# Performance work log

Hardware: AMD Instinct MI355X
Metric: run time of the kernel (lower is better)

Reference implementation:

```python
import jax, jax.numpy as jnp
import numpy as np
import math

N_HEADS = 8

def setup_inputs() -> dict:
    key = jax.random.key(0)
    qkv = jax.random.normal(key, (4, 1536, 2048), dtype=jnp.float32)
    return {"qkv": qkv}

def reference(qkv):
    bs, width, length = qkv.shape
    ch = width // (3 * N_HEADS)
    # reshape to [bs*n_heads, 3*ch, length] then split into q, k, v
    qkv_h = qkv.reshape(bs * N_HEADS, 3 * ch, length)
    q = qkv_h[:, :ch]
    k = qkv_h[:, ch:2 * ch]
    v = qkv_h[:, 2 * ch:]
    scale = 1.0 / math.sqrt(math.sqrt(ch))
    # scores: [B*H, T, S]
    weight = jnp.einsum('bct,bcs->bts', q * scale, k * scale)
    weight = jax.nn.softmax(weight.astype(jnp.float32), axis=-1).astype(weight.dtype)
    a = jnp.einsum('bts,bcs->bct', weight, v)  # [B*H, ch, T]
    return a.reshape(bs, N_HEADS * ch, length)
```

## Files before the change

### kernel.cpp

```cpp
#include <hip/hip_runtime.h>
#include <hip/hip_bf16.h>

typedef __attribute__((ext_vector_type(8))) short bf16x8;
typedef __attribute__((ext_vector_type(8))) unsigned short u16x8;
typedef __attribute__((ext_vector_type(4))) float f32x4;
typedef __attribute__((ext_vector_type(16))) float f32x16;

#define SEQ 2048
#define NBH 32
#define QSCALE 0.1803368801111204f

#if __has_builtin(__builtin_amdgcn_exp2f)
#define EXP2(x) __builtin_amdgcn_exp2f(x)
#else
#define EXP2(x) exp2f(x)
#endif

__device__ __forceinline__ unsigned short bfc(float f) {
  union { __hip_bfloat16 h; unsigned short u; } v;
  v.h = __float2bfloat16(f);
  return v.u;
}

__device__ __forceinline__ void gl_lds16(const void* g, void* l) {
  __builtin_amdgcn_global_load_lds((__attribute__((address_space(1))) void*)g,
                                   (__attribute__((address_space(3))) void*)l, 16, 0, 0);
}

__global__ __launch_bounds__(256)
void prep_kernel(const float* __restrict__ qkv, unsigned short* __restrict__ ws) {
  const int tid = threadIdx.x;
  const int b = blockIdx.x;
  if (b < 4096) {
    int gid = b * 256 + tid;
    int sec = gid >> 19;
    int r = gid & 524287;
    int bh = r >> 14;
    int rr = r & 16383;
    int cc = rr >> 11;
    int t = rr & 2047;
    const float* src = qkv + ((size_t)(bh >> 3) * 1536 + (bh & 7) * 192 + sec * 64 + cc * 8) * SEQ + t;
    const float scale = sec ? 1.0f : QSCALE;
    u16x8 o;
    #pragma unroll
    for (int e = 0; e < 8; ++e) o[e] = bfc(src[(size_t)e * SEQ] * scale);
    unsigned short* dst = ws + ((size_t)sec * NBH * SEQ + (size_t)bh * SEQ + t) * 64;
    *(u16x8*)(dst + ((cc ^ (t & 7)) * 8)) = o;
  } else {
    int cid = (b - 4096) * 256 + tid;
    int bh = cid >> 14;
    int rr = cid & 16383;
    int c = rr >> 8;
    int cc = rr & 255;
    int grp = cc >> 3, sub = cc & 7;
    const float* src = qkv + ((size_t)(bh >> 3) * 1536 + (bh & 7) * 192 + 128 + c) * SEQ + cc * 8;
    float4 a = *(const float4*)(src);
    float4 bv = *(const float4*)(src + 4);
    u16x8 o;
    o[0] = bfc(a.x); o[1] = bfc(a.y); o[2] = bfc(a.z); o[3] = bfc(a.w);
    o[4] = bfc(bv.x); o[5] = bfc(bv.y); o[6] = bfc(bv.z); o[7] = bfc(bv.w);
    unsigned short* dst = ws + (size_t)2 * NBH * SEQ * 64 +
                          ((size_t)bh * 64 + c) * SEQ + grp * 64 + ((sub ^ (c & 7)) * 8);
    *(u16x8*)dst = o;
  }
}

__global__ __launch_bounds__(256, 2)
void attn_main(const unsigned short* __restrict__ ws, float* __restrict__ out) {
  const int bid = blockIdx.x;
  const int bh = (bid & 7) + 8 * ((bid >> 3) >> 4);
  const int tile = (bid >> 3) & 15;
  const int t0 = tile * 128;

  const unsigned short* Qws = ws + ((size_t)bh * SEQ + t0) * 64;
  const unsigned short* Kws = ws + (size_t)NBH * SEQ * 64 + (size_t)bh * SEQ * 64;
  const unsigned short* Vws = ws + (size_t)2 * NBH * SEQ * 64 + (size_t)bh * 64 * SEQ;
  float* __restrict__ outb = out + (size_t)bh * 64 * SEQ;

  __shared__ __align__(16) char smem[32768];
  unsigned short* KtB = (unsigned short*)smem;
  unsigned short* VtB = (unsigned short*)(smem + 16384);

  const int tid = threadIdx.x;
  const int w = tid >> 6;
  const int ts = w & 1;
  const int sh = w >> 1;
  const int l = tid & 63;
  const int lw = l & 31;
  const int h = l >> 5;
  const int sw = lw & 7;

  bf16x8 qB[2][4];
  #pragma unroll
  for (int tsub = 0; tsub < 2; ++tsub) {
    const int rloc = ts * 64 + tsub * 32 + lw;
    #pragma unroll
    for (int kc = 0; kc < 4; ++kc)
      qB[tsub][kc] = *(const bf16x8*)&Qws[rloc * 64 + (((2 * kc + h) ^ sw) * 8)];
  }

  const int vc = tid >> 3, vj = tid & 7;
  const int vc2 = vc + 32;

  gl_lds16(Kws + (size_t)tid * 8, &KtB[tid * 8]);
  gl_lds16(Kws + (size_t)(tid + 256) * 8, &KtB[(tid + 256) * 8]);
  gl_lds16(Vws + (size_t)vc * SEQ + vj * 8, &VtB[tid * 8]);
  gl_lds16(Vws + (size_t)vc2 * SEQ + vj * 8, &VtB[(tid + 256) * 8]);
  __syncthreads();

  f32x16 zero16;
  #pragma unroll
  for (int i = 0; i < 16; ++i) zero16[i] = 0.f;
  bf16x8 onesB;
  #pragma unroll
  for (int i = 0; i < 8; ++i) onesB[i] = (short)0x3F80;

  f32x16 accO[2][2];
  f32x16 psum[2];
  accO[0][0] = zero16; accO[0][1] = zero16;
  accO[1][0] = zero16; accO[1][1] = zero16;
  psum[0] = zero16; psum[1] = zero16;

  int cur = 0;
  #pragma unroll 1
  for (int it = 0; it < SEQ / 64; ++it) {
    {
      const int s1 = (it + 1) & 31;
      const unsigned short* kn = Kws + (size_t)s1 * 4096;
      unsigned short* kd = KtB + (cur ^ 1) * 4096;
      gl_lds16(kn + (size_t)tid * 8, &kd[tid * 8]);
      gl_lds16(kn + (size_t)(tid + 256) * 8, &kd[(tid + 256) * 8]);
      unsigned short* vd = VtB + (cur ^ 1) * 4096;
      gl_lds16(Vws + (size_t)vc * SEQ + s1 * 64 + vj * 8, &vd[tid * 8]);
      gl_lds16(Vws + (size_t)vc2 * SEQ + s1 * 64 + vj * 8, &vd[(tid + 256) * 8]);
    }

    const unsigned short* kb = KtB + cur * 4096;
    const unsigned short* vb = VtB + cur * 4096;

    f32x16 accS[2];
    #pragma unroll
    for (int kc = 0; kc < 4; ++kc) {
      bf16x8 ka = *(const bf16x8*)&kb[(sh * 32 + lw) * 64 + (((2 * kc + h) ^ sw) * 8)];
      #pragma unroll
      for (int tsub = 0; tsub < 2; ++tsub)
        accS[tsub] = __builtin_amdgcn_mfma_f32_32x32x16_bf16(
            ka, qB[tsub][kc], kc ? accS[tsub] : zero16, 0, 0, 0);
    }

    #pragma unroll
    for (int tsub = 0; tsub < 2; ++tsub)
      #pragma unroll
      for (int r = 0; r < 16; ++r) accS[tsub][r] = EXP2(accS[tsub][r]);

    bf16x8 pA[2][2];
    #pragma unroll
    for (int tsub = 0; tsub < 2; ++tsub) {
      unsigned int pk[8];
      #pragma unroll
      for (int wd = 0; wd < 8; ++wd)
        asm("v_cvt_pk_bf16_f32 %0, %1, %2"
            : "=v"(pk[wd]) : "v"(accS[tsub][2 * wd]), "v"(accS[tsub][2 * wd + 1]));
      #pragma unroll
      for (int a = 0; a < 2; ++a) {
        unsigned int x0 = pk[4 * a + 0], y0 = pk[4 * a + 2];
        unsigned int x1 = pk[4 * a + 1], y1 = pk[4 * a + 3];
        asm("v_permlane32_swap_b32 %0, %1" : "+v"(x0), "+v"(y0));
        asm("v_permlane32_swap_b32 %0, %1" : "+v"(x1), "+v"(y1));
        union { unsigned int u[4]; bf16x8 v; } uu;
        uu.u[0] = x0; uu.u[1] = x1; uu.u[2] = y0; uu.u[3] = y1;
        pA[tsub][a] = uu.v;
      }
    }

    #pragma unroll
    for (int tsub = 0; tsub < 2; ++tsub)
      #pragma unroll
      for (int ks = 0; ks < 2; ++ks)
        psum[tsub] = __builtin_amdgcn_mfma_f32_32x32x16_bf16(pA[tsub][ks], onesB, psum[tsub], 0, 0, 0);

    #pragma unroll
    for (int ch = 0; ch < 2; ++ch) {
      #pragma unroll
      for (int ks = 0; ks < 2; ++ks) {
        bf16x8 vB = *(const bf16x8*)&vb[(32 * ch + lw) * 64 + (((sh * 4 + 2 * ks + h) ^ sw) * 8)];
        #pragma unroll
        for (int tsub = 0; tsub < 2; ++tsub)
          accO[tsub][ch] = __builtin_amdgcn_mfma_f32_32x32x16_bf16(pA[tsub][ks], vB, accO[tsub][ch], 0, 0, 0);
      }
    }

    __syncthreads();
    cur ^= 1;
  }

  float* red = (float*)smem;
  if (sh == 1) {
    #pragma unroll
    for (int tsub = 0; tsub < 2; ++tsub)
      #pragma unroll
      for (int ch = 0; ch < 2; ++ch)
        #pragma unroll
        for (int r = 0; r < 16; ++r)
          red[(((ts * 2 + tsub) * 2 + ch) * 16 + r) * 64 + l] = accO[tsub][ch][r];
  }
  __syncthreads();
  if (sh == 0) {
    #pragma unroll
    for (int tsub = 0; tsub < 2; ++tsub)
      #pragma unroll
      for (int ch = 0; ch < 2; ++ch)
        #pragma unroll
        for (int r = 0; r < 16; ++r)
          accO[tsub][ch][r] += red[(((ts * 2 + tsub) * 2 + ch) * 16 + r) * 64 + l];
  }
  __syncthreads();
  if (sh == 1) {
    #pragma unroll
    for (int tsub = 0; tsub < 2; ++tsub)
      #pragma unroll
      for (int r = 0; r < 16; ++r)
        red[((ts * 2 + tsub) * 16 + r) * 64 + l] = psum[tsub][r];
  }
  __syncthreads();
  if (sh == 0) {
    #pragma unroll
    for (int tsub = 0; tsub < 2; ++tsub) {
      float linv[16];
      #pragma unroll
      for (int r = 0; r < 16; ++r)
        linv[r] = 1.0f / (psum[tsub][r] + red[((ts * 2 + tsub) * 16 + r) * 64 + l]);
      #pragma unroll
      for (int ch = 0; ch < 2; ++ch) {
        #pragma unroll
        for (int r = 0; r < 16; ++r) {
          const int tg = t0 + ts * 64 + tsub * 32 + (r & 3) + 8 * (r >> 2) + 4 * h;
          outb[(size_t)(32 * ch + lw) * SEQ + tg] = accO[tsub][ch][r] * linv[r];
        }
      }
    }
  }
}

#define PAD 72
#define BTF 128
__device__ __forceinline__ unsigned short f2bf(float f) {
  union { float f; unsigned u; } v; v.f = f;
  return (unsigned short)((v.u + 0x7fffu + ((v.u >> 16) & 1u)) >> 16);
}

__global__ __launch_bounds__(512, 4)
void qkv_attn_fallback(const float* __restrict__ qkv, float* __restrict__ out) {
  const int bid = blockIdx.x;
  const int xcd = bid & 7;
  const int slot = bid >> 3;
  const int bh = xcd + 8 * (slot >> 4);
  const int tile = slot & 15;
  const int t0 = tile * BTF;

  const float* __restrict__ base = qkv + (size_t)((bh >> 3) * 1536 + (bh & 7) * 192) * SEQ;
  const float* __restrict__ qg = base;
  const float* __restrict__ kg = base + 64 * SEQ;
  const float* __restrict__ vg = base + 128 * SEQ;
  float* __restrict__ outb = out + (size_t)bh * 64 * SEQ;

  __shared__ __align__(16) unsigned short Qt[BTF * PAD];
  __shared__ __align__(16) unsigned short Kt[64 * PAD];
  __shared__ __align__(16) unsigned short Vt[64 * PAD];
  __shared__ __align__(16) unsigned short Pl[BTF * PAD];

  const int tid = threadIdx.x;
  const int w = tid >> 6;
  const int l = tid & 63;
  const int lr = l & 15;
  const int g = l >> 4;

  {
    const int cb = tid >> 5, tb = tid & 31;
    const int c0 = cb * 4, tt0 = tb * 4;
    const float* p = qg + c0 * SEQ + t0 + tt0;
    float4 r0 = *(const float4*)(p);
    float4 r1 = *(const float4*)(p + SEQ);
    float4 r2 = *(const float4*)(p + 2 * SEQ);
    float4 r3 = *(const float4*)(p + 3 * SEQ);
    const float s = 0.125f;
    ushort4 w0 = { f2bf(r0.x*s), f2bf(r1.x*s), f2bf(r2.x*s), f2bf(r3.x*s) };
    ushort4 w1 = { f2bf(r0.y*s), f2bf(r1.y*s), f2bf(r2.y*s), f2bf(r3.y*s) };
    ushort4 w2 = { f2bf(r0.z*s), f2bf(r1.z*s), f2bf(r2.z*s), f2bf(r3.z*s) };
    ushort4 w3 = { f2bf(r0.w*s), f2bf(r1.w*s), f2bf(r2.w*s), f2bf(r3.w*s) };
    *(ushort4*)&Qt[(tt0 + 0) * PAD + c0] = w0;
    *(ushort4*)&Qt[(tt0 + 1) * PAD + c0] = w1;
    *(ushort4*)&Qt[(tt0 + 2) * PAD + c0] = w2;
    *(ushort4*)&Qt[(tt0 + 3) * PAD + c0] = w3;
  }
  __syncthreads();

  bf16x8 qB0 = *(const bf16x8*)&Qt[(w * 16 + lr) * PAD + g * 8];
  bf16x8 qB1 = *(const bf16x8*)&Qt[(w * 16 + lr) * PAD + g * 8 + 32];

  f32x4 pv[4];
  #pragma unroll
  for (int i = 0; i < 4; ++i) pv[i] = (f32x4){0.f, 0.f, 0.f, 0.f};
  float mrun = -1e30f;
  float lsum = 0.f;

  for (int s0 = 0; s0 < SEQ; s0 += 64) {
    __syncthreads();
    {
      const int cb = tid >> 4, sb = tid & 15;
      const int c0 = cb * 2, sl = sb * 4;
      const float* p0 = kg + c0 * SEQ + s0 + sl;
      float4 a0 = *(const float4*)(p0);
      float4 a1 = *(const float4*)(p0 + SEQ);
      ushort2 y0 = { f2bf(a0.x), f2bf(a1.x) };
      ushort2 y1 = { f2bf(a0.y), f2bf(a1.y) };
      ushort2 y2 = { f2bf(a0.z), f2bf(a1.z) };
      ushort2 y3 = { f2bf(a0.w), f2bf(a1.w) };
      *(ushort2*)&Kt[(sl + 0) * PAD + c0] = y0;
      *(ushort2*)&Kt[(sl + 1) * PAD + c0] = y1;
      *(ushort2*)&Kt[(sl + 2) * PAD + c0] = y2;
      *(ushort2*)&Kt[(sl + 3) * PAD + c0] = y3;
    }
    {
      const int c = tid >> 3;
      const int sq = (tid & 7) * 8;
      const float* p0 = vg + c * SEQ + s0 + sq;
      float4 b0 = *(const float4*)(p0);
      float4 b1 = *(const float4*)(p0 + 4);
      ushort4 z0 = { f2bf(b0.x), f2bf(b0.y), f2bf(b0.z), f2bf(b0.w) };
      ushort4 z1 = { f2bf(b1.x), f2bf(b1.y), f2bf(b1.z), f2bf(b1.w) };
      *(ushort4*)&Vt[c * PAD + sq] = z0;
      *(ushort4*)&Vt[c * PAD + sq + 4] = z1;
    }
    __syncthreads();

    f32x4 acc[4];
    #pragma unroll
    for (int i = 0; i < 4; ++i) acc[i] = (f32x4){0.f, 0.f, 0.f, 0.f};
    #pragma unroll
    for (int ch = 0; ch < 2; ++ch) {
      bf16x8 qb = ch ? qB1 : qB0;
      #pragma unroll
      for (int sub = 0; sub < 4; ++sub) {
        bf16x8 ka = *(const bf16x8*)&Kt[(sub * 16 + lr) * PAD + g * 8 + 32 * ch];
        acc[sub] = __builtin_amdgcn_mfma_f32_16x16x32_bf16(ka, qb, acc[sub], 0, 0, 0);
      }
    }

    float pmax = -1e30f;
    #pragma unroll
    for (int sub = 0; sub < 4; ++sub)
      #pragma unroll
      for (int r = 0; r < 4; ++r) pmax = fmaxf(pmax, acc[sub][r]);
    pmax = fmaxf(pmax, __shfl_xor(pmax, 16));
    pmax = fmaxf(pmax, __shfl_xor(pmax, 32));
    const float mnew = fmaxf(mrun, pmax);
    const float alpha = __expf(mrun - mnew);
    float rsum = 0.f;
    #pragma unroll
    for (int sub = 0; sub < 4; ++sub) {
      #pragma unroll
      for (int r = 0; r < 4; ++r) {
        float p = __expf(acc[sub][r] - mnew);
        acc[sub][r] = p;
        rsum += p;
      }
    }
    rsum += __shfl_xor(rsum, 16);
    rsum += __shfl_xor(rsum, 32);
    lsum = lsum * alpha + rsum;
    mrun = mnew;

    #pragma unroll
    for (int sub = 0; sub < 4; ++sub) {
      ushort4 pw = { f2bf(acc[sub][0]), f2bf(acc[sub][1]), f2bf(acc[sub][2]), f2bf(acc[sub][3]) };
      *(ushort4*)&Pl[(w * 16 + lr) * PAD + sub * 16 + g * 4] = pw;
    }

    {
      const int sbase = (l & 48) + g * 4;
      #pragma unroll
      for (int r = 0; r < 4; ++r) {
        float ar = __shfl(alpha, sbase + r, 64);
        #pragma unroll
        for (int cs = 0; cs < 4; ++cs) pv[cs][r] *= ar;
      }
    }

    bf16x8 pA0 = *(const bf16x8*)&Pl[(w * 16 + lr) * PAD + g * 8];
    bf16x8 pA1 = *(const bf16x8*)&Pl[(w * 16 + lr) * PAD + g * 8 + 32];
    #pragma unroll
    for (int cs = 0; cs < 4; ++cs) {
      bf16x8 v0 = *(const bf16x8*)&Vt[(cs * 16 + lr) * PAD + g * 8];
      bf16x8 v1 = *(const bf16x8*)&Vt[(cs * 16 + lr) * PAD + g * 8 + 32];
      pv[cs] = __builtin_amdgcn_mfma_f32_16x16x32_bf16(pA0, v0, pv[cs], 0, 0, 0);
      pv[cs] = __builtin_amdgcn_mfma_f32_16x16x32_bf16(pA1, v1, pv[cs], 0, 0, 0);
    }
  }

  {
    const int sbase = (l & 48) + g * 4;
    float linv[4];
    #pragma unroll
    for (int r = 0; r < 4; ++r) linv[r] = 1.0f / __shfl(lsum, sbase + r, 64);
    #pragma unroll
    for (int cs = 0; cs < 4; ++cs) {
      #pragma unroll
      for (int r = 0; r < 4; ++r) {
        outb[(cs * 16 + lr) * SEQ + t0 + w * 16 + g * 4 + r] = pv[cs][r] * linv[r];
      }
    }
  }
}

extern "C" void kernel_launch(void* const* d_in, const int* in_sizes, int n_in,
                              void* d_out, int out_size, void* d_ws, size_t ws_size,
                              hipStream_t stream) {
  const float* qkv = (const float*)d_in[0];
  float* out = (float*)d_out;
  const size_t need = (size_t)3 * NBH * SEQ * 64 * sizeof(unsigned short);
  if (ws_size >= need) {
    unsigned short* ws = (unsigned short*)d_ws;
    prep_kernel<<<dim3(6144), dim3(256), 0, stream>>>(qkv, ws);
    attn_main<<<dim3(512), dim3(256), 0, stream>>>(ws, out);
  } else {
    qkv_attn_fallback<<<dim3(512), dim3(512), 0, stream>>>(qkv, out);
  }
}
```

Before: 61.12 us.

## Pre-pack K and V in MFMA fragment order and load directly to registers

The prep kernel now writes K and V into a layout ordered by the MFMA operand fragments each lane consumes. The main kernel then loads K and V straight from global memory into registers, with K prefetched one step ahead, instead of double-buffering them through LDS. This removes the LDS staging, the per-iteration __syncthreads, and the LDS reads. In exchange every wave fetches its own operands from global/L2 with no sharing through LDS, and the V loads are not prefetched, so global latency can be exposed inside the loop.

```diff
diff --git a/kernel.cpp b/kernel.cpp
--- a/kernel.cpp
+++ b/kernel.cpp
@@ -20,11 +20,6 @@
   union { __hip_bfloat16 h; unsigned short u; } v;
   v.h = __float2bfloat16(f);
   return v.u;
-}
-
-__device__ __forceinline__ void gl_lds16(const void* g, void* l) {
-  __builtin_amdgcn_global_load_lds((__attribute__((address_space(1))) void*)g,
-                                   (__attribute__((address_space(3))) void*)l, 16, 0, 0);
 }
 
 __global__ __launch_bounds__(256)
@@ -44,24 +39,34 @@
     u16x8 o;
     #pragma unroll
     for (int e = 0; e < 8; ++e) o[e] = bfc(src[(size_t)e * SEQ] * scale);
-    unsigned short* dst = ws + ((size_t)sec * NBH * SEQ + (size_t)bh * SEQ + t) * 64;
-    *(u16x8*)(dst + ((cc ^ (t & 7)) * 8)) = o;
+    if (sec == 0) {
+      unsigned short* dst = ws + ((size_t)bh * SEQ + t) * 64;
+      *(u16x8*)(dst + ((cc ^ (t & 7)) * 8)) = o;
+    } else {
+      const int tile = t >> 6, shh = (t >> 5) & 1, lww = t & 31;
+      const int kc = cc >> 1, hh = cc & 1;
+      unsigned short* dst = ws + (size_t)NBH * SEQ * 64 + (size_t)bh * SEQ * 64;
+      const int idx = ((tile * 2 + shh) * 4 + kc) * 64 + hh * 32 + lww;
+      *(u16x8*)(dst + (size_t)idx * 8) = o;
+    }
   } else {
     int cid = (b - 4096) * 256 + tid;
     int bh = cid >> 14;
     int rr = cid & 16383;
     int c = rr >> 8;
     int cc = rr & 255;
-    int grp = cc >> 3, sub = cc & 7;
+    int tile = cc >> 3, sub = cc & 7;
     const float* src = qkv + ((size_t)(bh >> 3) * 1536 + (bh & 7) * 192 + 128 + c) * SEQ + cc * 8;
     float4 a = *(const float4*)(src);
     float4 bv = *(const float4*)(src + 4);
     u16x8 o;
     o[0] = bfc(a.x); o[1] = bfc(a.y); o[2] = bfc(a.z); o[3] = bfc(a.w);
     o[4] = bfc(bv.x); o[5] = bfc(bv.y); o[6] = bfc(bv.z); o[7] = bfc(bv.w);
-    unsigned short* dst = ws + (size_t)2 * NBH * SEQ * 64 +
-                          ((size_t)bh * 64 + c) * SEQ + grp * 64 + ((sub ^ (c & 7)) * 8);
-    *(u16x8*)dst = o;
+    const int shh = sub >> 2, ks = (sub >> 1) & 1, hh = sub & 1;
+    const int ch = c >> 5, lww = c & 31;
+    unsigned short* dst = ws + (size_t)2 * NBH * SEQ * 64 + (size_t)bh * SEQ * 64;
+    const int idx = (((tile * 2 + shh) * 2 + ch) * 2 + ks) * 64 + hh * 32 + lww;
+    *(u16x8*)(dst + (size_t)idx * 8) = o;
   }
 }
 
@@ -69,17 +74,15 @@
 void attn_main(const unsigned short* __restrict__ ws, float* __restrict__ out) {
   const int bid = blockIdx.x;
   const int bh = (bid & 7) + 8 * ((bid >> 3) >> 4);
-  const int tile = (bid >> 3) & 15;
-  const int t0 = tile * 128;
+  const int tile0 = (bid >> 3) & 15;
+  const int t0 = tile0 * 128;
 
   const unsigned short* Qws = ws + ((size_t)bh * SEQ + t0) * 64;
-  const unsigned short* Kws = ws + (size_t)NBH * SEQ * 64 + (size_t)bh * SEQ * 64;
-  const unsigned short* Vws = ws + (size_t)2 * NBH * SEQ * 64 + (size_t)bh * 64 * SEQ;
+  const unsigned short* Kf = ws + (size_t)NBH * SEQ * 64 + (size_t)bh * SEQ * 64;
+  const unsigned short* Vf = ws + (size_t)2 * NBH * SEQ * 64 + (size_t)bh * SEQ * 64;
   float* __restrict__ outb = out + (size_t)bh * 64 * SEQ;
 
-  __shared__ __align__(16) char smem[32768];
-  unsigned short* KtB = (unsigned short*)smem;
-  unsigned short* VtB = (unsigned short*)(smem + 16384);
+  __shared__ __align__(16) float red[8192];
 
   const int tid = threadIdx.x;
   const int w = tid >> 6;
@@ -99,15 +102,6 @@
       qB[tsub][kc] = *(const bf16x8*)&Qws[rloc * 64 + (((2 * kc + h) ^ sw) * 8)];
   }
 
-  const int vc = tid >> 3, vj = tid & 7;
-  const int vc2 = vc + 32;
-
-  gl_lds16(Kws + (size_t)tid * 8, &KtB[tid * 8]);
-  gl_lds16(Kws + (size_t)(tid + 256) * 8, &KtB[(tid + 256) * 8]);
-  gl_lds16(Vws + (size_t)vc * SEQ + vj * 8, &VtB[tid * 8]);
-  gl_lds16(Vws + (size_t)vc2 * SEQ + vj * 8, &VtB[(tid + 256) * 8]);
-  __syncthreads();
-
   f32x16 zero16;
   #pragma unroll
   for (int i = 0; i < 16; ++i) zero16[i] = 0.f;
@@ -121,31 +115,34 @@
   accO[1][0] = zero16; accO[1][1] = zero16;
   psum[0] = zero16; psum[1] = zero16;
 
-  int cur = 0;
+  bf16x8 ka[4];
+  #pragma unroll
+  for (int kc = 0; kc < 4; ++kc)
+    ka[kc] = *(const bf16x8*)&Kf[(size_t)((sh * 4 + kc) * 64 + l) * 8];
+
   #pragma unroll 1
   for (int it = 0; it < SEQ / 64; ++it) {
+    bf16x8 kan[4];
     {
-      const int s1 = (it + 1) & 31;
-      const unsigned short* kn = Kws + (size_t)s1 * 4096;
-      unsigned short* kd = KtB + (cur ^ 1) * 4096;
-      gl_lds16(kn + (size_t)tid * 8, &kd[tid * 8]);
-      gl_lds16(kn + (size_t)(tid + 256) * 8, &kd[(tid + 256) * 8]);
-      unsigned short* vd = VtB + (cur ^ 1) * 4096;
-      gl_lds16(Vws + (size_t)vc * SEQ + s1 * 64 + vj * 8, &vd[tid * 8]);
-      gl_lds16(Vws + (size_t)vc2 * SEQ + s1 * 64 + vj * 8, &vd[(tid + 256) * 8]);
-    }
-
-    const unsigned short* kb = KtB + cur * 4096;
-    const unsigned short* vb = VtB + cur * 4096;
+      const int itn = (it + 1) & 31;
+      #pragma unroll
+      for (int kc = 0; kc < 4; ++kc)
+        kan[kc] = *(const bf16x8*)&Kf[(size_t)(((itn * 2 + sh) * 4 + kc) * 64 + l) * 8];
+    }
+    bf16x8 vB[2][2];
+    #pragma unroll
+    for (int ch = 0; ch < 2; ++ch)
+      #pragma unroll
+      for (int ks = 0; ks < 2; ++ks)
+        vB[ch][ks] = *(const bf16x8*)&Vf[(size_t)(((((it * 2 + sh) * 2 + ch) * 2 + ks)) * 64 + l) * 8];
 
     f32x16 accS[2];
     #pragma unroll
     for (int kc = 0; kc < 4; ++kc) {
-      bf16x8 ka = *(const bf16x8*)&kb[(sh * 32 + lw) * 64 + (((2 * kc + h) ^ sw) * 8)];
       #pragma unroll
       for (int tsub = 0; tsub < 2; ++tsub)
         accS[tsub] = __builtin_amdgcn_mfma_f32_32x32x16_bf16(
-            ka, qB[tsub][kc], kc ? accS[tsub] : zero16, 0, 0, 0);
+            ka[kc], qB[tsub][kc], kc ? accS[tsub] : zero16, 0, 0, 0);
     }
 
     #pragma unroll
@@ -183,18 +180,15 @@
     for (int ch = 0; ch < 2; ++ch) {
       #pragma unroll
       for (int ks = 0; ks < 2; ++ks) {
-        bf16x8 vB = *(const bf16x8*)&vb[(32 * ch + lw) * 64 + (((sh * 4 + 2 * ks + h) ^ sw) * 8)];
         #pragma unroll
         for (int tsub = 0; tsub < 2; ++tsub)
-          accO[tsub][ch] = __builtin_amdgcn_mfma_f32_32x32x16_bf16(pA[tsub][ks], vB, accO[tsub][ch], 0, 0, 0);
-      }
-    }
-
-    __syncthreads();
-    cur ^= 1;
-  }
-
-  float* red = (float*)smem;
+          accO[tsub][ch] = __builtin_amdgcn_mfma_f32_32x32x16_bf16(pA[tsub][ks], vB[ch][ks], accO[tsub][ch], 0, 0, 0);
+      }
+    }
+
+    ka[0] = kan[0]; ka[1] = kan[1]; ka[2] = kan[2]; ka[3] = kan[3];
+  }
+
   if (sh == 1) {
     #pragma unroll
     for (int tsub = 0; tsub < 2; ++tsub)
```

Result: slower. 65.01 us (+6.4%).
